# Kernel tuning notes

Measured on AMD Instinct MI355X. Metric: run time of the kernel, lower is better.

Reference implementation:

```python
import jax, jax.numpy as jnp
import numpy as np

WINDOW = 16      # window_size[0]
LANDM_H = 8      # closest_square_factors(64) = (8, 8)
LANDM_W = 8
MAX_VAL = 5.0
PINV_ITERS = 6


def activ(x):
    # ExpLinearAfterThreshold: exp(clamp(x, max=5)) + relu(x - 5)
    return jnp.exp(jnp.minimum(x, MAX_VAL)) + jax.nn.relu(x - MAX_VAL)


def pool_landmarks(x):
    # x: [B, H, N, d] with N = WINDOW*WINDOW.
    B, H, N, d = x.shape
    kh, kw = WINDOW // LANDM_H, WINDOW // LANDM_W
    x = x.reshape(B, H, LANDM_H, kh, LANDM_W, kw, d)
    return x.mean(axis=(3, 5)).reshape(B, H, LANDM_H * LANDM_W, d)  # [B, H, L, d]


def moore_penrose_pinv(x, iters=PINV_ITERS):
    # x: [B, H, L, L]
    abs_x = jnp.abs(x)
    col = abs_x.sum(axis=-1)
    row = abs_x.sum(axis=-2)
    z = jnp.swapaxes(x, -1, -2) / (jnp.max(col) * jnp.max(row) + 1e-15)
    I = jnp.eye(x.shape[-1], dtype=x.dtype)
    for _ in range(iters):
        xz = x @ z
        z = 0.25 * z @ (13.0 * I - xz @ (15.0 * I - xz @ (7.0 * I - xz)))
    return z


def setup_inputs() -> dict:
    key = jax.random.key(0)
    kq, kk, kv = jax.random.split(key, 3)
    shape = (256, 16, 256, 64)  # [B_, num_heads, window^2, head_dim]
    q = jax.random.normal(kq, shape, dtype=jnp.float32)
    k = jax.random.normal(kk, shape, dtype=jnp.float32)
    v = jax.random.normal(kv, shape, dtype=jnp.float32)
    return {"q": q, "k": k, "v": v}


def reference(q, k, v):
    # q, k, v: [B, H, N, d]
    q_m = pool_landmarks(q)  # [B, H, L, d]
    k_m = pool_landmarks(k)  # [B, H, L, d]

    temp = activ(jnp.einsum('bhld,bhmd->bhlm', q_m, k_m))   # [B, H, L, L]
    pinv = moore_penrose_pinv(temp, PINV_ITERS)              # [B, H, L, L]

    # kernel(q_m, k) @ [v | 1]  -> [B, H, L, d+1]
    v1 = jnp.concatenate([v, jnp.ones_like(v[..., :1])], axis=-1)
    kv = jnp.einsum('bhln,bhne->bhle', activ(jnp.einsum('bhld,bhnd->bhln', q_m, k)), v1)

    # kernel(q, k_m) @ pinv @ kv  -> [B, H, N, d+1]
    qk = activ(jnp.einsum('bhnd,bhld->bhnl', q, k_m))        # [B, H, N, L]
    prod = jnp.einsum('bhnl,bhle->bhne', qk @ pinv, kv)

    return prod[..., :-1] / (prod[..., -1:] + 1e-12)
```

## Files before the change

kernel.cpp:

```cpp
#include <hip/hip_runtime.h>
#include <math.h>


#define G_TOT 4096
#define TPB_R 256
#define TPB_M 1024
typedef _Float16 f16;
typedef __attribute__((ext_vector_type(2))) _Float16 f16x2;
typedef __attribute__((ext_vector_type(4))) _Float16 f16x4;
typedef __attribute__((ext_vector_type(8))) _Float16 f16x8;
typedef __attribute__((ext_vector_type(4))) float f32x4;
typedef __attribute__((ext_vector_type(16))) float f32x16;

#define NPLANES 16
#define SMEM_BYTES (NPLANES * 4096 * 2 + 64 * 4)

#define LSCALE 2048.0f
#define LINV   (1.0f / 2048.0f)
#define ZS     1024.0f
#define ZINV   (1.0f / 1024.0f)

struct HL { f16 h, l; };
__device__ __forceinline__ HL split2(float v) {
    HL r;
    r.h = (f16)v;
    r.l = (f16)((v - (float)r.h) * LSCALE);
    return r;
}
__device__ __forceinline__ float join2(f16 h, f16 l) {
    return (float)h + (float)l * LINV;
}
__device__ __forceinline__ int swi(int r, int c) {
    return (r << 6) + (c ^ ((r & 7) << 3));
}
__device__ __forceinline__ float activ_f(float x) {
    return __expf(fminf(x, 5.0f)) + fmaxf(x - 5.0f, 0.0f);
}
__device__ __forceinline__ float activ_r(float x) {
    return expf(fminf(x, 5.0f)) + fmaxf(x - 5.0f, 0.0f);
}
__device__ __forceinline__ void split_w(f16* Ph, f16* Pl, int r, int c, float v) {
    HL s = split2(v);
    const int o = swi(r, c);
    Ph[o] = s.h;
    Pl[o] = s.l;
}
__device__ __forceinline__ f16x2 mk2(f16 a, f16 b) { f16x2 r; r[0]=a; r[1]=b; return r; }
__device__ __forceinline__ f16x4 mk4(f16 a, f16 b, f16 c, f16 d) { f16x4 r; r[0]=a;r[1]=b;r[2]=c;r[3]=d; return r; }
__device__ __forceinline__ f32x4 z4() { f32x4 z = {0.f,0.f,0.f,0.f}; return z; }
__device__ __forceinline__ f32x16 z16() {
    f32x16 z;
#pragma unroll
    for (int i = 0; i < 16; ++i) z[i] = 0.f;
    return z;
}

struct Frag { f16x8 h[2], l[2]; };

__device__ __forceinline__ Frag ld_frag(const f16* __restrict__ Ph,
                                        const f16* __restrict__ Pl,
                                        int row, int kg) {
    Frag f;
    const int base = row << 6, x = (row & 7) << 3;
#pragma unroll
    for (int s = 0; s < 2; ++s) {
        const int o = base + ((((s << 5) + (kg << 3))) ^ x);
        f.h[s] = *(const f16x8*)(Ph + o);
        f.l[s] = *(const f16x8*)(Pl + o);
    }
    return f;
}

__device__ __forceinline__ f32x4 mm16_rr(const Frag& A, const Frag& B, f32x4 acc) {
    f32x4 ax = z4();
#pragma unroll
    for (int s = 0; s < 2; ++s) {
        acc = __builtin_amdgcn_mfma_f32_16x16x32_f16(A.h[s], B.h[s], acc, 0, 0, 0);
        ax  = __builtin_amdgcn_mfma_f32_16x16x32_f16(A.h[s], B.l[s], ax, 0, 0, 0);
        ax  = __builtin_amdgcn_mfma_f32_16x16x32_f16(A.l[s], B.h[s], ax, 0, 0, 0);
    }
    acc += ax * LINV;
    return acc;
}

__device__ __forceinline__ void wfrag_rm(f16* Ph, f16* Pl, int Rb, int C, const float* v) {
#pragma unroll
    for (int m = 0; m < 4; ++m) split_w(Ph, Pl, Rb + m, C, v[m]);
}
__device__ __forceinline__ void wfrag_t(f16* Ph, f16* Pl, int Rb, int C, const float* v) {
    const int o = swi(C, Rb);
    HL s0 = split2(v[0]), s1 = split2(v[1]), s2 = split2(v[2]), s3 = split2(v[3]);
    *(f16x4*)(Ph + o) = mk4(s0.h, s1.h, s2.h, s3.h);
    *(f16x4*)(Pl + o) = mk4(s0.l, s1.l, s2.l, s3.l);
}

__device__ __forceinline__ void wr_rm(float4 vv, f16* Ph, f16* Pl, int t) {
    const int r = t >> 4, c4 = (t & 15) << 2;
    const int o = swi(r, c4);
    HL s0 = split2(vv.x), s1 = split2(vv.y), s2 = split2(vv.z), s3 = split2(vv.w);
    *(f16x4*)(Ph + o) = mk4(s0.h, s1.h, s2.h, s3.h);
    *(f16x4*)(Pl + o) = mk4(s0.l, s1.l, s2.l, s3.l);
}
__device__ __forceinline__ void ld_vt(const float* __restrict__ src, int t,
                                      float2& va, float2& vb) {
    const int n0 = (t >> 5) << 1, e0 = (t & 31) << 1;
    va = *(const float2*)(src + (size_t)n0 * 64 + e0);
    vb = *(const float2*)(src + (size_t)(n0 + 1) * 64 + e0);
}
__device__ __forceinline__ void wr_vt(float2 va, float2 vb, f16* Ph, f16* Pl, int t) {
    const int n0 = (t >> 5) << 1, e0 = (t & 31) << 1;
    HL ax = split2(va.x), ay = split2(va.y), bx = split2(vb.x), by = split2(vb.y);
    const int o0 = swi(e0, n0), o1 = swi(e0 + 1, n0);
    *(f16x2*)(Ph + o0) = mk2(ax.h, bx.h);
    *(f16x2*)(Pl + o0) = mk2(ax.l, bx.l);
    *(f16x2*)(Ph + o1) = mk2(ay.h, by.h);
    *(f16x2*)(Pl + o1) = mk2(ay.l, by.l);
}
__device__ __forceinline__ void pool_global1024(const float* __restrict__ src,
                                                f16* Ph, f16* Pl, int t) {
    const int L = t >> 4, d0 = (t & 15) << 2;
    const int nb = ((L >> 3) << 5) + ((L & 7) << 1);
    const float* p = src + (size_t)nb * 64 + d0;
    float4 a = *(const float4*)p;
    float4 b = *(const float4*)(p + 64);
    float4 c = *(const float4*)(p + 1024);
    float4 d = *(const float4*)(p + 1088);
    HL s0 = split2(0.25f * (a.x + b.x + c.x + d.x));
    HL s1 = split2(0.25f * (a.y + b.y + c.y + d.y));
    HL s2 = split2(0.25f * (a.z + b.z + c.z + d.z));
    HL s3 = split2(0.25f * (a.w + b.w + c.w + d.w));
    const int o = swi(L, d0);
    *(f16x4*)(Ph + o) = mk4(s0.h, s1.h, s2.h, s3.h);
    *(f16x4*)(Pl + o) = mk4(s0.l, s1.l, s2.l, s3.l);
}
__device__ __forceinline__ void pool_lds512(const f16* Kh, const f16* Kl,
                                            f16* Ph, f16* Pl, int t, int tt) {
    const int ll = t >> 5, d0 = (t & 31) << 1;
    const int rb = ((ll >> 3) << 5) + ((ll & 7) << 1);
    float s0 = 0.f, s1 = 0.f;
#pragma unroll
    for (int rr = 0; rr < 4; ++rr) {
        const int r = rb + (rr & 1) + ((rr >> 1) << 4);
        const int o = swi(r, d0);
        f16x2 h = *(const f16x2*)(Kh + o);
        f16x2 l = *(const f16x2*)(Kl + o);
        s0 += join2(h[0], l[0]);
        s1 += join2(h[1], l[1]);
    }
    const int L = (tt << 4) + ll;
    HL p0 = split2(0.25f * s0), p1 = split2(0.25f * s1);
    const int o = swi(L, d0);
    *(f16x2*)(Ph + o) = mk2(p0.h, p1.h);
    *(f16x2*)(Pl + o) = mk2(p0.l, p1.l);
}

__device__ __forceinline__ f32x16 mm64q(const f16* __restrict__ Ah, const f16* __restrict__ Al,
                                        const f16* __restrict__ Bh, const f16* __restrict__ Bl,
                                        int lane, int wr, int wc, f32x16 acc) {
    const int cl = lane & 31, hh = lane >> 5;
    const int ar = (wr << 5) + cl, br = (wc << 5) + cl;
    const int abase = ar << 6, axor = (ar & 7) << 3;
    const int bbase = br << 6, bxor = (br & 7) << 3;
    f32x16 ax1 = z16();
    f32x16 ax2 = z16();
#pragma unroll
    for (int ks = 0; ks < 4; ++ks) {
        const int k0 = (ks << 4) + (hh << 3);
        const int ao = abase + (k0 ^ axor);
        const int bo = bbase + (k0 ^ bxor);
        f16x8 a_h = *(const f16x8*)(Ah + ao);
        f16x8 a_l = *(const f16x8*)(Al + ao);
        f16x8 b_h = *(const f16x8*)(Bh + bo);
        f16x8 b_l = *(const f16x8*)(Bl + bo);
        acc = __builtin_amdgcn_mfma_f32_32x32x16_f16(a_h, b_h, acc, 0, 0, 0);
        ax1 = __builtin_amdgcn_mfma_f32_32x32x16_f16(a_h, b_l, ax1, 0, 0, 0);
        ax2 = __builtin_amdgcn_mfma_f32_32x32x16_f16(a_l, b_h, ax2, 0, 0, 0);
    }
    acc += (ax1 + ax2) * LINV;
    return acc;
}
__device__ __forceinline__ void pool_global_r(const float* __restrict__ src,
                                              f16* Ph, f16* Pl, int t) {
    const int ll = t >> 4, d0 = (t & 15) << 2;
    const int rb = ((ll >> 3) << 5) + ((ll & 7) << 1);
#pragma unroll
    for (int tt = 0; tt < 4; ++tt) {
        const float* p = src + (size_t)((tt << 6) + rb) * 64 + d0;
        float4 a = *(const float4*)p;
        float4 b = *(const float4*)(p + 64);
        float4 c = *(const float4*)(p + 1024);
        float4 d = *(const float4*)(p + 1088);
        const int L = (tt << 4) + ll;
        split_w(Ph, Pl, L, d0 + 0, 0.25f * (a.x + b.x + c.x + d.x));
        split_w(Ph, Pl, L, d0 + 1, 0.25f * (a.y + b.y + c.y + d.y));
        split_w(Ph, Pl, L, d0 + 2, 0.25f * (a.z + b.z + c.z + d.z));
        split_w(Ph, Pl, L, d0 + 3, 0.25f * (a.w + b.w + c.w + d.w));
    }
}

#define WAVE_SUM32(v)            \
    v += __shfl_xor(v, 1);       \
    v += __shfl_xor(v, 2);       \
    v += __shfl_xor(v, 4);       \
    v += __shfl_xor(v, 8);       \
    v += __shfl_xor(v, 16);

__global__ void k_init(float* ws) {
    if (threadIdx.x < 2) ws[threadIdx.x] = 0.0f;
}

__global__ __launch_bounds__(TPB_R) void k_reduce(const float* __restrict__ q,
                                                  const float* __restrict__ k,
                                                  float* __restrict__ ws) {
    __shared__ f16 pls[4 * 4096];
    __shared__ float rowS[64], colS[64];
    const int t = threadIdx.x, g = blockIdx.x;
    const int lane = t & 63, wv = t >> 6, wr = wv >> 1, wc = wv & 1;
    const int cl = lane & 31, hh = lane >> 5;
    if (t < 64) rowS[t] = 0.f;
    else if (t < 128) colS[t - 64] = 0.f;
    pool_global_r(q + (size_t)g * 16384, pls, pls + 4096, t);
    pool_global_r(k + (size_t)g * 16384, pls + 8192, pls + 12288, t);
    __syncthreads();
    f32x16 a = mm64q(pls, pls + 4096, pls + 8192, pls + 12288, lane, wr, wc, z16());
    float colp = 0.f;
#pragma unroll
    for (int m = 0; m < 16; ++m) {
        float x = activ_r(a[m]);
        const int R = (wr << 5) + (m & 3) + ((m >> 2) << 3) + (hh << 2);
        float vs = x;
        WAVE_SUM32(vs)
        if (cl == 0) atomicAdd(&rowS[R], vs);
        colp += x;
    }
    colp += __shfl_xor(colp, 32);
    if (hh == 0) atomicAdd(&colS[(wc << 5) + cl], colp);
    __syncthreads();
    if (t < 64) {
        float vmx = rowS[t];
        for (int off = 1; off < 64; off <<= 1) vmx = fmaxf(vmx, __shfl_xor(vmx, off));
        if (t == 0) atomicMax((int*)ws, __float_as_int(vmx));
    } else if (t < 128) {
        float vmx = colS[t - 64];
        for (int off = 1; off < 64; off <<= 1) vmx = fmaxf(vmx, __shfl_xor(vmx, off));
        if (t == 64) atomicMax(((int*)ws) + 1, __float_as_int(vmx));
    }
}

__global__ __launch_bounds__(TPB_M, 4) void k_main(const float* __restrict__ q,
                                                   const float* __restrict__ k,
                                                   const float* __restrict__ v,
                                                   const float* __restrict__ ws,
                                                   float* __restrict__ out) {
    extern __shared__ f16 smu[];
    float* kv1 = (float*)(smu + NPLANES * 4096);
    const int t = threadIdx.x, g = blockIdx.x;
    const int lane = t & 63, w = t >> 6;
    const int ti = w & 3, tj = w >> 2;
    const int fr = lane & 15, kg = lane >> 4;
    const int arow = (ti << 4) + fr;
    const int brow = (tj << 4) + fr;
    const int C = brow;
    const int Rb = (ti << 4) + (kg << 2);
    const float* Gq = q + (size_t)g * 16384;
    const float* Gk = k + (size_t)g * 16384;
    const float* Gv = v + (size_t)g * 16384;
    float* og = out + (size_t)g * 16384;

    f16* Xh  = smu +  0 * 4096; f16* Xl  = smu +  1 * 4096;
    f16* SAh = smu +  2 * 4096; f16* SAl = smu +  3 * 4096;
    f16* SBh = smu +  4 * 4096; f16* SBl = smu +  5 * 4096;
    f16* KMh = smu +  6 * 4096; f16* KMl = smu +  7 * 4096;
    f16* SCh = smu +  8 * 4096; f16* SCl = smu +  9 * 4096;
    f16* KVh = smu + 10 * 4096; f16* KVl = smu + 11 * 4096;
    f16* Z0rh= smu + 12 * 4096; f16* Z0rl= smu + 13 * 4096;
    f16* Z0th= smu + 14 * 4096; f16* Z0tl= smu + 15 * 4096;

    Frag fOnes;
    {
        f16x8 one8, zer8;
#pragma unroll
        for (int i = 0; i < 8; ++i) { one8[i] = (f16)1.0f; zer8[i] = (f16)0.0f; }
        fOnes.h[0] = one8; fOnes.h[1] = one8;
        fOnes.l[0] = zer8; fOnes.l[1] = zer8;
    }

    pool_global1024(Gq, Z0rh, Z0rl, t);
    {
        float4 kreg = *(const float4*)(Gk + (size_t)t * 4);
        float2 va, vb; ld_vt(Gv, t, va, vb);
        wr_rm(kreg, SAh, SAl, t);
        wr_vt(va, vb, SBh, SBl, t);
    }
    __syncthreads();

    Frag fQM = ld_frag(Z0rh, Z0rl, arow, kg);

    f32x4 kva = z4();
    f32x4 kva1 = z4();
    for (int tt = 0; tt < 4; ++tt) {
        f16* vch = (tt & 1) ? Xh : SBh;  f16* vcl = (tt & 1) ? Xl : SBl;
        f16* vnh = (tt & 1) ? SBh : Xh;  f16* vnl = (tt & 1) ? SBl : Xl;
        float4 kregN; float2 vaN, vbN;
        if (tt < 3) {
            kregN = *(const float4*)(Gk + (size_t)(tt + 1) * 4096 + (size_t)t * 4);
            ld_vt(Gv + (size_t)(tt + 1) * 4096, t, vaN, vbN);
        }
        if (t < 512) pool_lds512(SAh, SAl, KMh, KMl, t, tt);
        {
            Frag bK = ld_frag(SAh, SAl, brow, kg);
            f32x4 s = mm16_rr(fQM, bK, z4());
            float sv[4];
#pragma unroll
            for (int m = 0; m < 4; ++m) sv[m] = activ_f(s[m]);
            wfrag_rm(SCh, SCl, Rb, C, sv);
        }
        if (tt < 3) wr_vt(vaN, vbN, vnh, vnl, t);
        __syncthreads();
        {
            Frag aS = ld_frag(SCh, SCl, arow, kg);
            Frag bV = ld_frag(vch, vcl, brow, kg);
            kva  = mm16_rr(aS, bV, kva);
            kva1 = mm16_rr(aS, fOnes, kva1);
        }
        if (tt < 3) wr_rm(kregN, SAh, SAl, t);
        __syncthreads();
    }

    {
        float kvv[4] = {kva[0], kva[1], kva[2], kva[3]};
        wfrag_t(KVh, KVl, Rb, C, kvv);
        Frag fKMb = ld_frag(KMh, KMl, brow, kg);
        f32x4 x0 = mm16_rr(fQM, fKMb, z4());
        const float scale = ZS / (ws[0] * ws[1] + 1e-15f);
        float xv[4], zv[4];
#pragma unroll
        for (int m = 0; m < 4; ++m) { xv[m] = activ_f(x0[m]); zv[m] = xv[m] * scale; }
        wfrag_rm(Xh, Xl, Rb, C, xv);
        wfrag_t (Z0rh, Z0rl, Rb, C, zv);
        wfrag_rm(Z0th, Z0tl, Rb, C, zv);
        if (tj == 0 && fr == 0) {
#pragma unroll
            for (int m = 0; m < 4; ++m) kv1[Rb + m] = kva1[m];
        }
    }
    __syncthreads();

    Frag fX = ld_frag(Xh, Xl, arow, kg);
    f16 *zrh = Z0rh, *zrl = Z0rl, *zth = Z0th, *ztl = Z0tl;
    f16 *nrh = SAh,  *nrl = SAl,  *nth = SCh,  *ntl = SCl;
#pragma unroll
    for (int it = 0; it < 6; ++it) {
        Frag bz = ld_frag(zth, ztl, brow, kg);
        f32x4 a1 = mm16_rr(fX, bz, z4());
        float t1k[4];
#pragma unroll
        for (int m = 0; m < 4; ++m) t1k[m] = a1[m] * ZINV;
        wfrag_rm(nrh, nrl, Rb, C, t1k);
        wfrag_t (nth, ntl, Rb, C, t1k);
        __syncthreads();
        Frag aT1 = ld_frag(nrh, nrl, arow, kg);
        Frag bT1 = ld_frag(nth, ntl, brow, kg);
        f32x4 a2 = mm16_rr(aT1, bT1, z4());
        float t2k[4];
#pragma unroll
        for (int m = 0; m < 4; ++m) t2k[m] = a2[m];
        wfrag_rm(Xh, Xl, Rb, C, t2k);
        __syncthreads();
        Frag aT2 = ld_frag(Xh, Xl, arow, kg);
        f32x4 a3 = mm16_rr(aT2, bT1, z4());
        float ov[4];
#pragma unroll
        for (int m = 0; m < 4; ++m) {
            const int R = Rb + m;
            ov[m] = ((R == C) ? 13.f : 0.f) - 15.f * t1k[m] + 7.f * t2k[m] - a3[m];
        }
        wfrag_t(SBh, SBl, Rb, C, ov);
        __syncthreads();
        Frag aZ = ld_frag(zrh, zrl, arow, kg);
        Frag bO = ld_frag(SBh, SBl, brow, kg);
        f32x4 a4 = mm16_rr(aZ, bO, z4());
        float zk[4];
#pragma unroll
        for (int m = 0; m < 4; ++m) zk[m] = 0.25f * a4[m];
        wfrag_rm(nrh, nrl, Rb, C, zk);
        wfrag_t (nth, ntl, Rb, C, zk);
        __syncthreads();
        f16* tp;
        tp = zrh; zrh = nrh; nrh = tp;  tp = zrl; zrl = nrl; nrl = tp;
        tp = zth; zth = nth; nth = tp;  tp = ztl; ztl = ntl; ntl = tp;
    }

    Frag fKM = ld_frag(KMh, KMl, brow, kg);
    Frag fZt = ld_frag(Z0th, Z0tl, brow, kg);
    Frag fKV = ld_frag(KVh, KVl, brow, kg);
    Frag fKv1;
#pragma unroll
    for (int s = 0; s < 2; ++s) {
        const float* kp = kv1 + (s << 5) + (kg << 3);
        float4 A = *(const float4*)kp;
        float4 B = *(const float4*)(kp + 4);
        HL s0 = split2(A.x), s1 = split2(A.y), s2 = split2(A.z), s3 = split2(A.w);
        HL s4 = split2(B.x), s5 = split2(B.y), s6 = split2(B.z), s7 = split2(B.w);
        f16x8 h, l;
        h[0]=s0.h; h[1]=s1.h; h[2]=s2.h; h[3]=s3.h; h[4]=s4.h; h[5]=s5.h; h[6]=s6.h; h[7]=s7.h;
        l[0]=s0.l; l[1]=s1.l; l[2]=s2.l; l[3]=s3.l; l[4]=s4.l; l[5]=s5.l; l[6]=s6.l; l[7]=s7.l;
        fKv1.h[s] = h; fKv1.l[s] = l;
    }
    float4 qp0, qp1, qp2, qp3;
#define LOAD_Q(tt_)                                                              \
    {                                                                            \
        const float* rp = Gq + (size_t)(((tt_) << 6) + arow) * 64 + (kg << 3);   \
        qp0 = *(const float4*)(rp);      qp1 = *(const float4*)(rp + 4);         \
        qp2 = *(const float4*)(rp + 32); qp3 = *(const float4*)(rp + 36);        \
    }
    LOAD_Q(0)
    for (int tt = 0; tt < 4; ++tt) {
        {
            Frag aQ;
            {
                HL s0 = split2(qp0.x), s1 = split2(qp0.y), s2 = split2(qp0.z), s3 = split2(qp0.w);
                HL s4 = split2(qp1.x), s5 = split2(qp1.y), s6 = split2(qp1.z), s7 = split2(qp1.w);
                f16x8 h, l;
                h[0]=s0.h; h[1]=s1.h; h[2]=s2.h; h[3]=s3.h; h[4]=s4.h; h[5]=s5.h; h[6]=s6.h; h[7]=s7.h;
                l[0]=s0.l; l[1]=s1.l; l[2]=s2.l; l[3]=s3.l; l[4]=s4.l; l[5]=s5.l; l[6]=s6.l; l[7]=s7.l;
                aQ.h[0] = h; aQ.l[0] = l;
                HL t0 = split2(qp2.x), t1 = split2(qp2.y), t2 = split2(qp2.z), t3 = split2(qp2.w);
                HL t4 = split2(qp3.x), t5 = split2(qp3.y), t6 = split2(qp3.z), t7 = split2(qp3.w);
                f16x8 h2, l2;
                h2[0]=t0.h; h2[1]=t1.h; h2[2]=t2.h; h2[3]=t3.h; h2[4]=t4.h; h2[5]=t5.h; h2[6]=t6.h; h2[7]=t7.h;
                l2[0]=t0.l; l2[1]=t1.l; l2[2]=t2.l; l2[3]=t3.l; l2[4]=t4.l; l2[5]=t5.l; l2[6]=t6.l; l2[7]=t7.l;
                aQ.h[1] = h2; aQ.l[1] = l2;
            }
            f32x4 q0 = mm16_rr(aQ, fKM, z4());
            float qv[4];
#pragma unroll
            for (int m = 0; m < 4; ++m) qv[m] = activ_f(q0[m]);
            wfrag_rm(SCh, SCl, Rb, C, qv);
        }
        __syncthreads();
        {
            Frag aK = ld_frag(SCh, SCl, arow, kg);
            f32x4 w0 = mm16_rr(aK, fZt, z4());
            float wv[4];
#pragma unroll
            for (int m = 0; m < 4; ++m) wv[m] = w0[m] * ZINV;
            wfrag_rm(SBh, SBl, Rb, C, wv);
        }
        if (tt < 3) LOAD_Q(tt + 1)
        __syncthreads();
        {
            Frag aW = ld_frag(SBh, SBl, arow, kg);
            f32x4 p0 = mm16_rr(aW, fKV, z4());
            f32x4 d4 = mm16_rr(aW, fKv1, z4());
#pragma unroll
            for (int m = 0; m < 4; ++m) {
                const int R = Rb + m;
                const float inv = 1.0f / (d4[m] + 1e-12f);
                og[(size_t)((tt << 6) + R) * 64 + C] = p0[m] * inv;
            }
        }
        __syncthreads();
    }
#undef LOAD_Q
}

extern "C" void kernel_launch(void* const* d_in, const int* in_sizes, int n_in,
                              void* d_out, int out_size, void* d_ws, size_t ws_size,
                              hipStream_t stream) {
    const float* q = (const float*)d_in[0];
    const float* k = (const float*)d_in[1];
    const float* v = (const float*)d_in[2];
    float* out = (float*)d_out;
    float* ws  = (float*)d_ws;
    (void)in_sizes; (void)n_in; (void)out_size; (void)ws_size;

    hipFuncSetAttribute((const void*)k_main,
                        hipFuncAttributeMaxDynamicSharedMemorySize, SMEM_BYTES);

    k_init<<<1, 64, 0, stream>>>(ws);
    k_reduce<<<G_TOT, TPB_R, 0, stream>>>(q, k, ws);
    k_main<<<G_TOT, TPB_M, SMEM_BYTES, stream>>>(q, k, v, ws, out);
}
```

Before: 794.3 us.

## Restructure pinv iteration algebra and software-pipeline output tiles to cut barriers

Rewrites each Newton-Schulz step as z' = 0.25*(13z - 15 zX + (zX)(7X - X^2)), with X = xz. This computes two matmuls in parallel per phase and drops from four barriers to three per iteration. The output stage is unrolled and software-pipelined so the QK, W and PROD stages of consecutive tiles share barriers, using rotating shared buffers. The kv1 row is stored pre-split into f16 hi/lo so it can be loaded directly. The rewritten algebra changes rounding order in the split-f16 emulation, which risks some accuracy and adds register pressure.

```diff
diff --git a/kernel.cpp b/kernel.cpp
--- a/kernel.cpp
+++ b/kernel.cpp
@@ -13,7 +13,7 @@
 typedef __attribute__((ext_vector_type(16))) float f32x16;
 
 #define NPLANES 16
-#define SMEM_BYTES (NPLANES * 4096 * 2 + 64 * 4)
+#define SMEM_BYTES (NPLANES * 4096 * 2 + 256)
 
 #define LSCALE 2048.0f
 #define LINV   (1.0f / 2048.0f)
@@ -253,7 +253,8 @@
                                                    const float* __restrict__ ws,
                                                    float* __restrict__ out) {
     extern __shared__ f16 smu[];
-    float* kv1 = (float*)(smu + NPLANES * 4096);
+    f16* kv1h = smu + NPLANES * 4096;
+    f16* kv1l = kv1h + 64;
     const int t = threadIdx.x, g = blockIdx.x;
     const int lane = t & 63, w = t >> 6;
     const int ti = w & 3, tj = w >> 2;
@@ -341,72 +342,52 @@
         wfrag_rm(Z0th, Z0tl, Rb, C, zv);
         if (tj == 0 && fr == 0) {
 #pragma unroll
-            for (int m = 0; m < 4; ++m) kv1[Rb + m] = kva1[m];
+            for (int m = 0; m < 4; ++m) {
+                HL s = split2(kva1[m]);
+                kv1h[Rb + m] = s.h;
+                kv1l[Rb + m] = s.l;
+            }
         }
     }
     __syncthreads();
 
     Frag fX = ld_frag(Xh, Xl, arow, kg);
-    f16 *zrh = Z0rh, *zrl = Z0rl, *zth = Z0th, *ztl = Z0tl;
-    f16 *nrh = SAh,  *nrl = SAl,  *nth = SCh,  *ntl = SCl;
 #pragma unroll
     for (int it = 0; it < 6; ++it) {
-        Frag bz = ld_frag(zth, ztl, brow, kg);
+        Frag bz = ld_frag(Z0th, Z0tl, brow, kg);
         f32x4 a1 = mm16_rr(fX, bz, z4());
         float t1k[4];
 #pragma unroll
         for (int m = 0; m < 4; ++m) t1k[m] = a1[m] * ZINV;
-        wfrag_rm(nrh, nrl, Rb, C, t1k);
-        wfrag_t (nth, ntl, Rb, C, t1k);
+        wfrag_rm(SAh, SAl, Rb, C, t1k);
+        wfrag_t (SCh, SCl, Rb, C, t1k);
         __syncthreads();
-        Frag aT1 = ld_frag(nrh, nrl, arow, kg);
-        Frag bT1 = ld_frag(nth, ntl, brow, kg);
-        f32x4 a2 = mm16_rr(aT1, bT1, z4());
-        float t2k[4];
-#pragma unroll
-        for (int m = 0; m < 4; ++m) t2k[m] = a2[m];
-        wfrag_rm(Xh, Xl, Rb, C, t2k);
+        Frag aM  = ld_frag(SAh, SAl, arow, kg);
+        Frag bMt = ld_frag(SCh, SCl, brow, kg);
+        f32x4 pP = mm16_rr(aM, bMt, z4());
+        Frag aZ  = ld_frag(Z0rh, Z0rl, arow, kg);
+        f32x4 wS = mm16_rr(aZ, bMt, z4());
+        float opv[4], wv[4];
+#pragma unroll
+        for (int m = 0; m < 4; ++m) { opv[m] = 7.f * t1k[m] - pP[m]; wv[m] = wS[m]; }
+        wfrag_t (Xh, Xl, Rb, C, opv);
+        wfrag_rm(SBh, SBl, Rb, C, wv);
         __syncthreads();
-        Frag aT2 = ld_frag(Xh, Xl, arow, kg);
-        f32x4 a3 = mm16_rr(aT2, bT1, z4());
-        float ov[4];
+        Frag aW  = ld_frag(SBh, SBl, arow, kg);
+        Frag bOP = ld_frag(Xh, Xl, brow, kg);
+        f32x4 yS = mm16_rr(aW, bOP, z4());
+        float zk[4];
 #pragma unroll
         for (int m = 0; m < 4; ++m) {
-            const int R = Rb + m;
-            ov[m] = ((R == C) ? 13.f : 0.f) - 15.f * t1k[m] + 7.f * t2k[m] - a3[m];
+            const int o = swi(Rb + m, C);
+            const float zs = join2(Z0rh[o], Z0rl[o]);
+            zk[m] = 0.25f * (13.f * zs - 15.f * wv[m] + yS[m]);
         }
-        wfrag_t(SBh, SBl, Rb, C, ov);
+        wfrag_rm(Z0rh, Z0rl, Rb, C, zk);
+        wfrag_t (Z0th, Z0tl, Rb, C, zk);
         __syncthreads();
-        Frag aZ = ld_frag(zrh, zrl, arow, kg);
-        Frag bO = ld_frag(SBh, SBl, brow, kg);
-        f32x4 a4 = mm16_rr(aZ, bO, z4());
-        float zk[4];
-#pragma unroll
-        for (int m = 0; m < 4; ++m) zk[m] = 0.25f * a4[m];
-        wfrag_rm(nrh, nrl, Rb, C, zk);
-        wfrag_t (nth, ntl, Rb, C, zk);
-        __syncthreads();
-        f16* tp;
-        tp = zrh; zrh = nrh; nrh = tp;  tp = zrl; zrl = nrl; nrl = tp;
-        tp = zth; zth = nth; nth = tp;  tp = ztl; ztl = ntl; ntl = tp;
-    }
-
-    Frag fKM = ld_frag(KMh, KMl, brow, kg);
-    Frag fZt = ld_frag(Z0th, Z0tl, brow, kg);
-    Frag fKV = ld_frag(KVh, KVl, brow, kg);
-    Frag fKv1;
-#pragma unroll
-    for (int s = 0; s < 2; ++s) {
-        const float* kp = kv1 + (s << 5) + (kg << 3);
-        float4 A = *(const float4*)kp;
-        float4 B = *(const float4*)(kp + 4);
-        HL s0 = split2(A.x), s1 = split2(A.y), s2 = split2(A.z), s3 = split2(A.w);
-        HL s4 = split2(B.x), s5 = split2(B.y), s6 = split2(B.z), s7 = split2(B.w);
-        f16x8 h, l;
-        h[0]=s0.h; h[1]=s1.h; h[2]=s2.h; h[3]=s3.h; h[4]=s4.h; h[5]=s5.h; h[6]=s6.h; h[7]=s7.h;
-        l[0]=s0.l; l[1]=s1.l; l[2]=s2.l; l[3]=s3.l; l[4]=s4.l; l[5]=s5.l; l[6]=s6.l; l[7]=s7.l;
-        fKv1.h[s] = h; fKv1.l[s] = l;
-    }
+    }
+
     float4 qp0, qp1, qp2, qp3;
 #define LOAD_Q(tt_)                                                              \
     {                                                                            \
@@ -414,55 +395,87 @@
         qp0 = *(const float4*)(rp);      qp1 = *(const float4*)(rp + 4);         \
         qp2 = *(const float4*)(rp + 32); qp3 = *(const float4*)(rp + 36);        \
     }
+#define BUILD_AQ(aQ_)                                                                          \
+    {                                                                                          \
+        HL s0 = split2(qp0.x), s1 = split2(qp0.y), s2 = split2(qp0.z), s3 = split2(qp0.w);     \
+        HL s4 = split2(qp1.x), s5 = split2(qp1.y), s6 = split2(qp1.z), s7 = split2(qp1.w);     \
+        f16x8 h, l;                                                                            \
+        h[0]=s0.h; h[1]=s1.h; h[2]=s2.h; h[3]=s3.h; h[4]=s4.h; h[5]=s5.h; h[6]=s6.h; h[7]=s7.h;\
+        l[0]=s0.l; l[1]=s1.l; l[2]=s2.l; l[3]=s3.l; l[4]=s4.l; l[5]=s5.l; l[6]=s6.l; l[7]=s7.l;\
+        aQ_.h[0] = h; aQ_.l[0] = l;                                                            \
+        HL t0 = split2(qp2.x), t1 = split2(qp2.y), t2 = split2(qp2.z), t3 = split2(qp2.w);     \
+        HL t4 = split2(qp3.x), t5 = split2(qp3.y), t6 = split2(qp3.z), t7 = split2(qp3.w);     \
+        f16x8 h2, l2;                                                                          \
+        h2[0]=t0.h; h2[1]=t1.h; h2[2]=t2.h; h2[3]=t3.h; h2[4]=t4.h; h2[5]=t5.h; h2[6]=t6.h; h2[7]=t7.h; \
+        l2[0]=t0.l; l2[1]=t1.l; l2[2]=t2.l; l2[3]=t3.l; l2[4]=t4.l; l2[5]=t5.l; l2[6]=t6.l; l2[7]=t7.l; \
+        aQ_.h[1] = h2; aQ_.l[1] = l2;                                                          \
+    }
+#define DO_QK(dsth, dstl)                                             \
+    {                                                                 \
+        Frag aQ; BUILD_AQ(aQ)                                         \
+        Frag bKM = ld_frag(KMh, KMl, brow, kg);                       \
+        f32x4 q0 = mm16_rr(aQ, bKM, z4());                            \
+        float qv[4];                                                  \
+        _Pragma("unroll")                                             \
+        for (int m = 0; m < 4; ++m) qv[m] = activ_f(q0[m]);           \
+        wfrag_rm(dsth, dstl, Rb, C, qv);                              \
+    }
+#define DO_W(srch, srcl, dsth, dstl)                                  \
+    {                                                                 \
+        Frag aK = ld_frag(srch, srcl, arow, kg);                      \
+        Frag bZt = ld_frag(Z0th, Z0tl, brow, kg);                     \
+        f32x4 w0 = mm16_rr(aK, bZt, z4());                            \
+        float wv2[4];                                                 \
+        _Pragma("unroll")                                             \
+        for (int m = 0; m < 4; ++m) wv2[m] = w0[m] * ZINV;            \
+        wfrag_rm(dsth, dstl, Rb, C, wv2);                             \
+    }
+#define DO_PROD(srch, srcl, tt_)                                      \
+    {                                                                 \
+        Frag aW2 = ld_frag(srch, srcl, arow, kg);                     \
+        Frag bKV = ld_frag(KVh, KVl, brow, kg);                       \
+        f32x4 p0 = mm16_rr(aW2, bKV, z4());                           \
+        Frag fk;                                                      \
+        _Pragma("unroll")                                             \
+        for (int s = 0; s < 2; ++s) {                                 \
+            const int o = (s << 5) + (kg << 3);                       \
+            fk.h[s] = *(const f16x8*)(kv1h + o);                      \
+            fk.l[s] = *(const f16x8*)(kv1l + o);                      \
+        }                                                             \
+        f32x4 d4 = mm16_rr(aW2, fk, z4());                            \
+        _Pragma("unroll")                                             \
+        for (int m = 0; m < 4; ++m) {                                 \
+            const int R = Rb + m;                                     \
+            og[(size_t)(((tt_) << 6) + R) * 64 + C] = p0[m] / (d4[m] + 1e-12f); \
+        }                                                             \
+    }
+
     LOAD_Q(0)
-    for (int tt = 0; tt < 4; ++tt) {
-        {
-            Frag aQ;
-            {
-                HL s0 = split2(qp0.x), s1 = split2(qp0.y), s2 = split2(qp0.z), s3 = split2(qp0.w);
-                HL s4 = split2(qp1.x), s5 = split2(qp1.y), s6 = split2(qp1.z), s7 = split2(qp1.w);
-                f16x8 h, l;
-                h[0]=s0.h; h[1]=s1.h; h[2]=s2.h; h[3]=s3.h; h[4]=s4.h; h[5]=s5.h; h[6]=s6.h; h[7]=s7.h;
-                l[0]=s0.l; l[1]=s1.l; l[2]=s2.l; l[3]=s3.l; l[4]=s4.l; l[5]=s5.l; l[6]=s6.l; l[7]=s7.l;
-                aQ.h[0] = h; aQ.l[0] = l;
-                HL t0 = split2(qp2.x), t1 = split2(qp2.y), t2 = split2(qp2.z), t3 = split2(qp2.w);
-                HL t4 = split2(qp3.x), t5 = split2(qp3.y), t6 = split2(qp3.z), t7 = split2(qp3.w);
-                f16x8 h2, l2;
-                h2[0]=t0.h; h2[1]=t1.h; h2[2]=t2.h; h2[3]=t3.h; h2[4]=t4.h; h2[5]=t5.h; h2[6]=t6.h; h2[7]=t7.h;
-                l2[0]=t0.l; l2[1]=t1.l; l2[2]=t2.l; l2[3]=t3.l; l2[4]=t4.l; l2[5]=t5.l; l2[6]=t6.l; l2[7]=t7.l;
-                aQ.h[1] = h2; aQ.l[1] = l2;
-            }
-            f32x4 q0 = mm16_rr(aQ, fKM, z4());
-            float qv[4];
-#pragma unroll
-            for (int m = 0; m < 4; ++m) qv[m] = activ_f(q0[m]);
-            wfrag_rm(SCh, SCl, Rb, C, qv);
-        }
-        __syncthreads();
-        {
-            Frag aK = ld_frag(SCh, SCl, arow, kg);
-            f32x4 w0 = mm16_rr(aK, fZt, z4());
-            float wv[4];
-#pragma unroll
-            for (int m = 0; m < 4; ++m) wv[m] = w0[m] * ZINV;
-            wfrag_rm(SBh, SBl, Rb, C, wv);
-        }
-        if (tt < 3) LOAD_Q(tt + 1)
-        __syncthreads();
-        {
-            Frag aW = ld_frag(SBh, SBl, arow, kg);
-            f32x4 p0 = mm16_rr(aW, fKV, z4());
-            f32x4 d4 = mm16_rr(aW, fKv1, z4());
-#pragma unroll
-            for (int m = 0; m < 4; ++m) {
-                const int R = Rb + m;
-                const float inv = 1.0f / (d4[m] + 1e-12f);
-                og[(size_t)((tt << 6) + R) * 64 + C] = p0[m] * inv;
-            }
-        }
-        __syncthreads();
-    }
+    DO_QK(SCh, SCl)
+    LOAD_Q(1)
+    __syncthreads();
+    DO_W(SCh, SCl, SBh, SBl)
+    DO_QK(SAh, SAl)
+    LOAD_Q(2)
+    __syncthreads();
+    DO_PROD(SBh, SBl, 0)
+    DO_W(SAh, SAl, Xh, Xl)
+    DO_QK(SCh, SCl)
+    LOAD_Q(3)
+    __syncthreads();
+    DO_PROD(Xh, Xl, 1)
+    DO_W(SCh, SCl, SBh, SBl)
+    DO_QK(SAh, SAl)
+    __syncthreads();
+    DO_PROD(SBh, SBl, 2)
+    DO_W(SAh, SAl, Xh, Xl)
+    __syncthreads();
+    DO_PROD(Xh, Xl, 3)
 #undef LOAD_Q
+#undef BUILD_AQ
+#undef DO_QK
+#undef DO_W
+#undef DO_PROD
 }
 
 extern "C" void kernel_launch(void* const* d_in, const int* in_sizes, int n_in,
```

New measurement: 758.7 us. 1.05x faster.
